# Optimization experiments

Hardware: AMD Instinct MI355X
Metric: run time of the kernel (lower is better)

Reference implementation:

```python
import jax, jax.numpy as jnp
import numpy as np

EPS = 1e-8

def _div(n, d):
    # div_with_small_value: d = d if d > eps else eps
    return n / jnp.where(d > EPS, d, EPS)

def _lstm_dir(x, Wih, Whh, bih, bhh):
    # x: (B, L, I) -> (hs (B, L, H), h_last (B, H))
    B, L, _ = x.shape
    H = Whh.shape[1]
    xg = jnp.einsum('bli,gi->blg', x, Wih) + bih + bhh  # (B, L, 4H)
    def step(carry, g):
        h, c = carry
        g = g + h @ Whh.T
        i, f, gg, o = jnp.split(g, 4, axis=-1)
        c = jax.nn.sigmoid(f) * c + jax.nn.sigmoid(i) * jnp.tanh(gg)
        h = jax.nn.sigmoid(o) * jnp.tanh(c)
        return (h, c), h
    init = (jnp.zeros((B, H), x.dtype), jnp.zeros((B, H), x.dtype))
    (hT, _), hs = jax.lax.scan(step, init, jnp.swapaxes(xg, 0, 1))
    return jnp.swapaxes(hs, 0, 1), hT

def _bilstm(x, pf, pb):
    fw, fwT = _lstm_dir(x, *pf)
    bw_r, bwT = _lstm_dir(x[:, ::-1], *pb)
    return fw, bw_r[:, ::-1], fwT, bwT

def _mp_full(v1, v2, w):
    # v1 (B,L,H); v2 (B,H) or (B,L,H); w (P,H) -> (B,L,P)
    wv1 = v1[:, :, None, :] * w                      # (B,L,P,H)
    if v2.ndim == 2:
        wv2 = v2[:, None, None, :] * w               # (B,1,P,H)
    else:
        wv2 = v2[:, :, None, :] * w                  # (B,L,P,H)
    num = jnp.sum(wv1 * wv2, -1)
    den = jnp.linalg.norm(wv1, axis=-1) * jnp.linalg.norm(wv2, axis=-1)
    return num / jnp.maximum(den, EPS)               # torch cosine_similarity eps

def _mp_pairwise(v1, v2, w):
    # v1 (B,L1,H), v2 (B,L2,H), w (P,H) -> (B,L1,L2,P)
    wv1 = w[None, :, None, :] * v1[:, None]          # (B,P,L1,H)
    wv2 = w[None, :, None, :] * v2[:, None]          # (B,P,L2,H)
    n = jnp.einsum('bpld,bpmd->bplm', wv1, wv2)
    d = jnp.linalg.norm(wv1, axis=-1)[..., :, None] * jnp.linalg.norm(wv2, axis=-1)[..., None, :]
    return jnp.transpose(_div(n, d), (0, 2, 3, 1))

def _attention(v1, v2):
    # cosine similarity matrix (B, L1, L2)
    n = jnp.einsum('bld,bmd->blm', v1, v2)
    d = jnp.linalg.norm(v1, axis=-1)[:, :, None] * jnp.linalg.norm(v2, axis=-1)[:, None, :]
    return _div(n, d)

def _forward(emb, cWih_f, cWhh_f, cbih_f, cbhh_f, cWih_b, cWhh_b, cbih_b, cbhh_b,
             aWih_f, aWhh_f, abih_f, abhh_f, aWih_b, aWhh_b, abih_b, abhh_b,
             mp_w1, mp_w2, mp_w3, mp_w4, mp_w5, mp_w6, mp_w7, mp_w8,
             fc1_W, fc1_b, fc2_W, fc2_b, text_a, text_b):
    p = emb[text_a]
    h = emb[text_b]
    cpf_p = (cWih_f, cWhh_f, cbih_f, cbhh_f)
    cpb_p = (cWih_b, cWhh_b, cbih_b, cbhh_b)
    con_p_fw, con_p_bw, _, _ = _bilstm(p, cpf_p, cpb_p)
    con_h_fw, con_h_bw, _, _ = _bilstm(h, cpf_p, cpb_p)
    # full matching
    mv_p_full_fw = _mp_full(con_p_fw, con_h_fw[:, -1], mp_w1)
    mv_p_full_bw = _mp_full(con_p_bw, con_h_bw[:, 0], mp_w2)
    mv_h_full_fw = _mp_full(con_h_fw, con_p_fw[:, -1], mp_w1)
    mv_h_full_bw = _mp_full(con_h_bw, con_p_bw[:, 0], mp_w2)
    # maxpool matching
    mv_max_fw = _mp_pairwise(con_p_fw, con_h_fw, mp_w3)
    mv_max_bw = _mp_pairwise(con_p_bw, con_h_bw, mp_w4)
    mv_p_max_fw = mv_max_fw.max(2); mv_p_max_bw = mv_max_bw.max(2)
    mv_h_max_fw = mv_max_fw.max(1); mv_h_max_bw = mv_max_bw.max(1)
    # attentive matching
    att_fw = _attention(con_p_fw, con_h_fw)          # (B,L1,L2)
    att_bw = _attention(con_p_bw, con_h_bw)
    att_h_fw = con_h_fw[:, None] * att_fw[..., None]     # (B,L1,L2,H)
    att_h_bw = con_h_bw[:, None] * att_bw[..., None]
    att_p_fw = con_p_fw[:, :, None] * att_fw[..., None]  # (B,L1,L2,H)
    att_p_bw = con_p_bw[:, :, None] * att_bw[..., None]
    att_mean_h_fw = _div(att_h_fw.sum(2), att_fw.sum(2, keepdims=True))
    att_mean_h_bw = _div(att_h_bw.sum(2), att_bw.sum(2, keepdims=True))
    att_mean_p_fw = _div(att_p_fw.sum(1), jnp.swapaxes(att_fw.sum(1, keepdims=True), 1, 2))
    att_mean_p_bw = _div(att_p_bw.sum(1), jnp.swapaxes(att_bw.sum(1, keepdims=True), 1, 2))
    mv_p_att_mean_fw = _mp_full(con_p_fw, att_mean_h_fw, mp_w5)
    mv_p_att_mean_bw = _mp_full(con_p_bw, att_mean_h_bw, mp_w6)
    mv_h_att_mean_fw = _mp_full(con_h_fw, att_mean_p_fw, mp_w5)
    mv_h_att_mean_bw = _mp_full(con_h_bw, att_mean_p_bw, mp_w6)
    att_max_h_fw = att_h_fw.max(2); att_max_h_bw = att_h_bw.max(2)
    att_max_p_fw = att_p_fw.max(1); att_max_p_bw = att_p_bw.max(1)
    mv_p_att_max_fw = _mp_full(con_p_fw, att_max_h_fw, mp_w7)
    mv_p_att_max_bw = _mp_full(con_p_bw, att_max_h_bw, mp_w8)
    mv_h_att_max_fw = _mp_full(con_h_fw, att_max_p_fw, mp_w7)
    mv_h_att_max_bw = _mp_full(con_h_bw, att_max_p_bw, mp_w8)
    mv_p = jnp.concatenate([mv_p_full_fw, mv_p_max_fw, mv_p_att_mean_fw, mv_p_att_max_fw,
                            mv_p_full_bw, mv_p_max_bw, mv_p_att_mean_bw, mv_p_att_max_bw], 2)
    mv_h = jnp.concatenate([mv_h_full_fw, mv_h_max_fw, mv_h_att_mean_fw, mv_h_att_max_fw,
                            mv_h_full_bw, mv_h_max_bw, mv_h_att_mean_bw, mv_h_att_max_bw], 2)
    apf = (aWih_f, aWhh_f, abih_f, abhh_f)
    apb = (aWih_b, aWhh_b, abih_b, abhh_b)
    _, _, p_fwT, p_bwT = _bilstm(mv_p, apf, apb)
    _, _, h_fwT, h_bwT = _bilstm(mv_h, apf, apb)
    x = jnp.concatenate([p_fwT, p_bwT, h_fwT, h_bwT], 1)  # (B, 4H)
    x = jnp.tanh(x @ fc1_W.T + fc1_b)
    return x @ fc2_W.T + fc2_b

def setup_inputs() -> dict:
    key = jax.random.key(0)
    ks = jax.random.split(key, 40)
    B, L, V, E, H, P = 16, 128, 30000, 300, 128, 4
    def n(i, shape, s=0.05):
        return jax.random.normal(ks[i], shape, jnp.float32) * s
    inp = {
        'text_a': jax.random.randint(ks[0], (B, L), 0, V, jnp.int32),
        'text_b': jax.random.randint(ks[1], (B, L), 0, V, jnp.int32),
        'emb': n(2, (V, E), 0.1),
        'cWih_f': n(3, (4*H, E)), 'cWhh_f': n(4, (4*H, H)), 'cbih_f': n(5, (4*H,)), 'cbhh_f': n(6, (4*H,)),
        'cWih_b': n(7, (4*H, E)), 'cWhh_b': n(8, (4*H, H)), 'cbih_b': n(9, (4*H,)), 'cbhh_b': n(10, (4*H,)),
        'aWih_f': n(11, (4*H, 8*P)), 'aWhh_f': n(12, (4*H, H)), 'abih_f': n(13, (4*H,)), 'abhh_f': n(14, (4*H,)),
        'aWih_b': n(15, (4*H, 8*P)), 'aWhh_b': n(16, (4*H, H)), 'abih_b': n(17, (4*H,)), 'abhh_b': n(18, (4*H,)),
        'fc1_W': n(19, (2*H, 4*H)), 'fc1_b': n(20, (2*H,)),
        'fc2_W': n(21, (2, 2*H)), 'fc2_b': n(22, (2,)),
    }
    for i in range(1, 9):
        inp[f'mp_w{i}'] = jax.random.uniform(ks[22 + i], (P, H), jnp.float32)
    return inp

def reference(text_a, text_b, emb, cWih_f, cWhh_f, cbih_f, cbhh_f, cWih_b, cWhh_b, cbih_b, cbhh_b,
              aWih_f, aWhh_f, abih_f, abhh_f, aWih_b, aWhh_b, abih_b, abhh_b,
              fc1_W, fc1_b, fc2_W, fc2_b, mp_w1, mp_w2, mp_w3, mp_w4, mp_w5, mp_w6, mp_w7, mp_w8):
    return _forward(emb, cWih_f, cWhh_f, cbih_f, cbhh_f, cWih_b, cWhh_b, cbih_b, cbhh_b,
                    aWih_f, aWhh_f, abih_f, abhh_f, aWih_b, aWhh_b, abih_b, abhh_b,
                    mp_w1, mp_w2, mp_w3, mp_w4, mp_w5, mp_w6, mp_w7, mp_w8,
                    fc1_W, fc1_b, fc2_W, fc2_b, text_a, text_b)
```

## Files before the change

kernel.cpp:

```cpp
#include <hip/hip_runtime.h>

#define B_ 16
#define L_ 128
#define ML_ 2048
#define E_ 300
#define H_ 128
#define G_ 512
#define EPSV 1e-8f

typedef const float* fp;
typedef __attribute__((ext_vector_type(2))) float f32x2;

__device__ __forceinline__ float sigm(float x) { return 1.f / (1.f + __expf(-x)); }
__device__ __forceinline__ float tanh_f(float x) {
  float e = __expf(-2.f * fabsf(x));
  float r = (1.f - e) / (1.f + e);
  return copysignf(r, x);
}
__device__ __forceinline__ float ddiv(float n, float d) {
  return n / (d > EPSV ? d : EPSV);
}
__device__ __forceinline__ void pkfma(f32x2& d, f32x2 a, f32x2 b) {
  asm("v_pk_fma_f32 %0, %1, %2, %0" : "+v"(d) : "v"(a), "v"(b));
}

__global__ __launch_bounds__(256) void k_proj(
    fp __restrict__ emb,
    const int* __restrict__ ta, const int* __restrict__ tb,
    fp Wf, fp Wb, fp bihf, fp bhhf, fp bihb, fp bhhb,
    float* __restrict__ xg)
{
  const int z = blockIdx.z;
  const int* txt = (z >> 1) ? tb : ta;
  fp W = (z & 1) ? Wb : Wf;
  fp bih = (z & 1) ? bihb : bihf;
  fp bhh = (z & 1) ? bhhb : bhhf;
  float* out = xg + (size_t)z * ML_ * G_;
  const int m0 = blockIdx.x * 64, n0 = blockIdx.y * 64;
  __shared__ float As[12][64];
  __shared__ float Bs[12][64];
  __shared__ int rowidx[64];
  const int tid = threadIdx.x;
  if (tid < 64) rowidx[tid] = txt[m0 + tid];
  __syncthreads();
  const int tm = tid >> 4, tn = tid & 15;
  float acc[4][4] = {};
  for (int k0 = 0; k0 < 300; k0 += 12) {
    for (int i = tid; i < 768; i += 256) {
      int m = i / 12, k = i - m * 12;
      As[k][m] = emb[(size_t)rowidx[m] * 300 + k0 + k];
    }
    for (int i = tid; i < 768; i += 256) {
      int n = i / 12, k = i - n * 12;
      Bs[k][n] = W[(size_t)(n0 + n) * 300 + k0 + k];
    }
    __syncthreads();
    #pragma unroll
    for (int k = 0; k < 12; ++k) {
      float4 a = *(const float4*)&As[k][tm * 4];
      float4 bv = *(const float4*)&Bs[k][tn * 4];
      float aa[4] = {a.x, a.y, a.z, a.w};
      #pragma unroll
      for (int i = 0; i < 4; ++i) {
        acc[i][0] = fmaf(aa[i], bv.x, acc[i][0]);
        acc[i][1] = fmaf(aa[i], bv.y, acc[i][1]);
        acc[i][2] = fmaf(aa[i], bv.z, acc[i][2]);
        acc[i][3] = fmaf(aa[i], bv.w, acc[i][3]);
      }
    }
    __syncthreads();
  }
  float biasv[4];
  #pragma unroll
  for (int j = 0; j < 4; ++j)
    biasv[j] = bih[n0 + tn * 4 + j] + bhh[n0 + tn * 4 + j];
  #pragma unroll
  for (int i = 0; i < 4; ++i) {
    float* row = out + (size_t)(m0 + tm * 4 + i) * G_ + n0 + tn * 4;
    #pragma unroll
    for (int j = 0; j < 4; ++j) row[j] = acc[i][j] + biasv[j];
  }
}

__global__ __launch_bounds__(512, 2) void k_lstm(
    fp __restrict__ xg, fp Whhf, fp Whhb, float* __restrict__ out)
{
  const int b = blockIdx.x, z = blockIdx.y, dir = z & 1;
  fp Whh = dir ? Whhb : Whhf;
  fp __restrict__ xgz = xg + ((size_t)z * ML_ + (size_t)b * L_) * G_;
  float* __restrict__ outz = out + ((size_t)z * ML_ + (size_t)b * L_) * H_;
  const int tid = threadIdx.x;
  const int wv = tid >> 6, l = tid & 63;
  const int kh = l & 3, rg = l >> 2;
  const int j = wv * 16 + rg;
  const int b0 = kh & 1, b1 = (kh >> 1) & 1;
  float4 wq[4][8];
  #pragma unroll
  for (int g = 0; g < 4; ++g) {
    const float4* p = (const float4*)(Whh + (size_t)(g * 128 + j) * H_ + kh * 32);
    #pragma unroll
    for (int q = 0; q < 8; ++q) wq[g][q] = p[q];
  }
  __shared__ float hs[2][128];
  if (tid < 128) hs[0][tid] = 0.f;
  float c = 0.f;
  const int pos0 = dir ? (L_ - 1) : 0;
  float xv = xgz[(size_t)pos0 * G_ + kh * 128 + j];
  __syncthreads();
  int cur = 0;
  for (int t = 0; t < L_; ++t) {
    const int pos = dir ? (L_ - 1 - t) : t;
    const int tnx = (t + 1 < L_) ? (t + 1) : t;
    const int posn = dir ? (L_ - 1 - tnx) : tnx;
    float xvn = xgz[(size_t)posn * G_ + kh * 128 + j];
    f32x2 a2[4];
    #pragma unroll
    for (int g = 0; g < 4; ++g) { a2[g].x = 0.f; a2[g].y = 0.f; }
    const float4* h4 = (const float4*)(&hs[cur][kh * 32]);
    #pragma unroll
    for (int q = 0; q < 8; ++q) {
      float4 hv = h4[q];
      f32x2 hlo; hlo.x = hv.x; hlo.y = hv.y;
      f32x2 hhi; hhi.x = hv.z; hhi.y = hv.w;
      #pragma unroll
      for (int g = 0; g < 4; ++g) {
        float4 wqv = wq[g][q];
        f32x2 wlo; wlo.x = wqv.x; wlo.y = wqv.y;
        f32x2 whi; whi.x = wqv.z; whi.y = wqv.w;
        pkfma(a2[g], wlo, hlo);
        pkfma(a2[g], whi, hhi);
      }
    }
    float pg0 = a2[0].x + a2[0].y;
    float pg1 = a2[1].x + a2[1].y;
    float pg2 = a2[2].x + a2[2].y;
    float pg3 = a2[3].x + a2[3].y;
    float sendA = b0 ? pg0 : pg1;
    float sendB = b0 ? pg2 : pg3;
    float keepA = b0 ? pg1 : pg0;
    float keepB = b0 ? pg3 : pg2;
    float uA = keepA + __shfl_xor(sendA, 1, 64);
    float uB = keepB + __shfl_xor(sendB, 1, 64);
    float mine  = b1 ? uB : uA;
    float send2 = b1 ? uA : uB;
    float tot = mine + __shfl_xor(send2, 2, 64);
    float pre = tot + xv;
    float act = (kh == 2) ? tanh_f(pre) : sigm(pre);
    float e1 = __shfl_xor(act, 1, 64);
    float e2 = __shfl_xor(act, 2, 64);
    float e3 = __shfl_xor(e1, 2, 64);
    float iv = (kh == 0) ? act : (kh == 1) ? e1 : (kh == 2) ? e2 : e3;
    float fv = (kh == 0) ? e1 : (kh == 1) ? act : (kh == 2) ? e3 : e2;
    float gv = (kh == 0) ? e2 : (kh == 1) ? e3 : (kh == 2) ? act : e1;
    float ov = (kh == 0) ? e3 : (kh == 1) ? e2 : (kh == 2) ? e1 : act;
    c = fmaf(fv, c, iv * gv);
    float hn = ov * tanh_f(c);
    const int nxt = cur ^ 1;
    if (kh == 0) {
      hs[nxt][j] = hn;
      outz[(size_t)pos * H_ + j] = hn;
    }
    asm volatile("s_waitcnt lgkmcnt(0)" ::: "memory");
    __builtin_amdgcn_s_barrier();
    cur = nxt; xv = xvn;
  }
}

__global__ __launch_bounds__(256) void k_att(
    fp __restrict__ con, fp w3, fp w4,
    float* __restrict__ att, float* __restrict__ ameanh, float* __restrict__ amaxh,
    float* __restrict__ pcpart, float* __restrict__ mv)
{
  const int b = blockIdx.x, dir = blockIdx.y, lt = blockIdx.z;
  const int l0 = lt * 32;
  fp __restrict__ cp = con + ((size_t)dir * B_ + b) * L_ * H_;
  fp __restrict__ ch = con + ((size_t)(2 + dir) * B_ + b) * L_ * H_;
  fp w = dir ? w4 : w3;
  float* __restrict__ attg = att + ((size_t)dir * B_ + b) * L_ * L_;
  __shared__ float cps[32][132];
  __shared__ float chs[32][132];
  __shared__ float w2s[4][128];
  __shared__ float attb[32][33];
  __shared__ float pcb[4][32][33];
  __shared__ float n0l[32], nql[4][32], n0m[32], nqm[4][32], asum_s[32];
  const int tid = threadIdx.x;
  for (int i = tid; i < 512; i += 256) {
    float wv = w[i];
    w2s[i >> 7][i & 127] = wv * wv;
  }
  for (int i = tid; i < 4096; i += 256)
    cps[i >> 7][i & 127] = cp[(size_t)(l0 + (i >> 7)) * H_ + (i & 127)];
  __syncthreads();
  for (int d = tid; d < 160; d += 256) {
    int l = d / 5, q = d - l * 5;
    const float4* vr = (const float4*)&cps[l][0];
    float s = 0.f;
    if (q == 0) {
      #pragma unroll 8
      for (int h4 = 0; h4 < 32; ++h4) {
        float4 v = vr[h4];
        s += v.x*v.x + v.y*v.y + v.z*v.z + v.w*v.w;
      }
      n0l[l] = sqrtf(s);
    } else {
      const float4* wr = (const float4*)&w2s[q - 1][0];
      #pragma unroll 8
      for (int h4 = 0; h4 < 32; ++h4) {
        float4 v = vr[h4]; float4 ww = wr[h4];
        s += v.x*v.x*ww.x + v.y*v.y*ww.y + v.z*v.z*ww.z + v.w*v.w*ww.w;
      }
      nql[q - 1][l] = sqrtf(s);
    }
  }
  const int tl = tid >> 3, t8 = tid & 7;
  float amean_acc[16], amax_acc[16];
  #pragma unroll
  for (int i = 0; i < 16; ++i) { amean_acc[i] = 0.f; amax_acc[i] = -3.4e38f; }
  float asum_reg = 0.f;
  float pmax_reg = -3.4e38f;
  for (int mc = 0; mc < 4; ++mc) {
    __syncthreads();
    for (int i = tid; i < 4096; i += 256)
      chs[i >> 7][i & 127] = ch[(size_t)(mc * 32 + (i >> 7)) * H_ + (i & 127)];
    __syncthreads();
    for (int d = tid; d < 160; d += 256) {
      int m = d / 5, q = d - m * 5;
      const float4* vr = (const float4*)&chs[m][0];
      float s = 0.f;
      if (q == 0) {
        #pragma unroll 8
        for (int h4 = 0; h4 < 32; ++h4) {
          float4 v = vr[h4];
          s += v.x*v.x + v.y*v.y + v.z*v.z + v.w*v.w;
        }
        n0m[m] = sqrtf(s);
      } else {
        const float4* wr = (const float4*)&w2s[q - 1][0];
        #pragma unroll 8
        for (int h4 = 0; h4 < 32; ++h4) {
          float4 v = vr[h4]; float4 ww = wr[h4];
          s += v.x*v.x*ww.x + v.y*v.y*ww.y + v.z*v.z*ww.z + v.w*v.w*ww.w;
        }
        nqm[q - 1][m] = sqrtf(s);
      }
    }
    __syncthreads();
    float a0[4], ap0[4], ap1[4], ap2[4], ap3[4];
    #pragma unroll
    for (int mm = 0; mm < 4; ++mm) { a0[mm]=0.f; ap0[mm]=0.f; ap1[mm]=0.f; ap2[mm]=0.f; ap3[mm]=0.f; }
    #pragma unroll 4
    for (int h4 = 0; h4 < 32; ++h4) {
      const float4 av = *(const float4*)&cps[tl][h4 * 4];
      const float4 q0 = *(const float4*)&w2s[0][h4 * 4];
      const float4 q1 = *(const float4*)&w2s[1][h4 * 4];
      const float4 q2 = *(const float4*)&w2s[2][h4 * 4];
      const float4 q3 = *(const float4*)&w2s[3][h4 * 4];
      #pragma unroll
      for (int mm = 0; mm < 4; ++mm) {
        const float4 cv = *(const float4*)&chs[t8 * 4 + mm][h4 * 4];
        float px = av.x * cv.x, py = av.y * cv.y, pz = av.z * cv.z, pw = av.w * cv.w;
        a0[mm] += (px + py) + (pz + pw);
        ap0[mm] += px * q0.x + py * q0.y + pz * q0.z + pw * q0.w;
        ap1[mm] += px * q1.x + py * q1.y + pz * q1.z + pw * q1.w;
        ap2[mm] += px * q2.x + py * q2.y + pz * q2.z + pw * q2.w;
        ap3[mm] += px * q3.x + py * q3.y + pz * q3.z + pw * q3.w;
      }
    }
    #pragma unroll
    for (int mm = 0; mm < 4; ++mm) {
      const int m = t8 * 4 + mm;
      float attv = ddiv(a0[mm], n0l[tl] * n0m[m]);
      attb[tl][m] = attv;
      attg[(size_t)(l0 + tl) * L_ + mc * 32 + m] = attv;
      pcb[0][tl][m] = ddiv(ap0[mm], nql[0][tl] * nqm[0][m]);
      pcb[1][tl][m] = ddiv(ap1[mm], nql[1][tl] * nqm[1][m]);
      pcb[2][tl][m] = ddiv(ap2[mm], nql[2][tl] * nqm[2][m]);
      pcb[3][tl][m] = ddiv(ap3[mm], nql[3][tl] * nqm[3][m]);
    }
    __syncthreads();
    for (int mq = 0; mq < 32; ++mq) {
      float avv = attb[tl][mq];
      const float4* cr = (const float4*)&chs[mq][t8 * 16];
      #pragma unroll
      for (int i = 0; i < 4; ++i) {
        float4 cv = cr[i];
        float t0 = avv * cv.x, t1 = avv * cv.y, t2 = avv * cv.z, t3 = avv * cv.w;
        amean_acc[4*i+0] += t0; amax_acc[4*i+0] = fmaxf(amax_acc[4*i+0], t0);
        amean_acc[4*i+1] += t1; amax_acc[4*i+1] = fmaxf(amax_acc[4*i+1], t1);
        amean_acc[4*i+2] += t2; amax_acc[4*i+2] = fmaxf(amax_acc[4*i+2], t2);
        amean_acc[4*i+3] += t3; amax_acc[4*i+3] = fmaxf(amax_acc[4*i+3], t3);
      }
    }
    if (tid < 32) {
      float s = 0.f;
      for (int mq = 0; mq < 32; ++mq) s += attb[tid][mq];
      asum_reg += s;
    }
    if (tid < 128) {
      const int p = tid >> 5, q = tid & 31;
      float mx = pmax_reg;
      for (int mq = 0; mq < 32; ++mq) mx = fmaxf(mx, pcb[p][q][mq]);
      pmax_reg = mx;
      float mx2 = -3.4e38f;
      for (int lq = 0; lq < 32; ++lq) mx2 = fmaxf(mx2, pcb[p][lq][q]);
      pcpart[((((size_t)dir * B_ + b) * 4 + lt) * 4 + p) * L_ + mc * 32 + q] = mx2;
    }
    __syncthreads();
  }
  if (tid < 32) asum_s[tid] = asum_reg;
  __syncthreads();
  {
    float den = asum_s[tl]; den = (den > EPSV) ? den : EPSV;
    const size_t base = (((size_t)dir * B_ + b) * L_ + l0 + tl) * H_ + t8 * 16;
    #pragma unroll
    for (int i = 0; i < 16; ++i) {
      ameanh[base + i] = amean_acc[i] / den;
      amaxh[base + i] = amax_acc[i];
    }
  }
  if (tid < 128) {
    const int p = tid >> 5, lq = tid & 31;
    mv[(size_t)(b * L_ + l0 + lq) * 32 + (dir ? 20 : 4) + p] = pmax_reg;
  }
}

__global__ __launch_bounds__(256) void k_col(
    fp __restrict__ con, fp __restrict__ att,
    fp __restrict__ pcpart,
    float* __restrict__ ameanp, float* __restrict__ amaxp, float* __restrict__ mv)
{
  const int b = blockIdx.x, dir = blockIdx.y, mt = blockIdx.z;
  const int m0 = mt * 32;
  fp __restrict__ cp = con + ((size_t)dir * B_ + b) * L_ * H_;
  fp __restrict__ attg = att + ((size_t)dir * B_ + b) * L_ * L_;
  __shared__ float atts[128][33];
  __shared__ float cpc[32][132];
  __shared__ float asum_s[32];
  const int tid = threadIdx.x;
  for (int i = tid; i < 4096; i += 256)
    atts[i >> 5][i & 31] = attg[(size_t)(i >> 5) * L_ + m0 + (i & 31)];
  __syncthreads();
  if (tid < 32) {
    float s = 0.f;
    for (int l = 0; l < 128; ++l) s += atts[l][tid];
    asum_s[tid] = s;
  }
  const int tm = tid >> 3, t8 = tid & 7;
  float mean_acc[16], max_acc[16];
  #pragma unroll
  for (int i = 0; i < 16; ++i) { mean_acc[i] = 0.f; max_acc[i] = -3.4e38f; }
  for (int lc = 0; lc < 4; ++lc) {
    __syncthreads();
    for (int i = tid; i < 4096; i += 256)
      cpc[i >> 7][i & 127] = cp[(size_t)(lc * 32 + (i >> 7)) * H_ + (i & 127)];
    __syncthreads();
    for (int lq = 0; lq < 32; ++lq) {
      float avv = atts[lc * 32 + lq][tm];
      const float4* cr = (const float4*)&cpc[lq][t8 * 16];
      #pragma unroll
      for (int i = 0; i < 4; ++i) {
        float4 cv = cr[i];
        float t0 = avv * cv.x, t1 = avv * cv.y, t2 = avv * cv.z, t3 = avv * cv.w;
        mean_acc[4*i+0] += t0; max_acc[4*i+0] = fmaxf(max_acc[4*i+0], t0);
        mean_acc[4*i+1] += t1; max_acc[4*i+1] = fmaxf(max_acc[4*i+1], t1);
        mean_acc[4*i+2] += t2; max_acc[4*i+2] = fmaxf(max_acc[4*i+2], t2);
        mean_acc[4*i+3] += t3; max_acc[4*i+3] = fmaxf(max_acc[4*i+3], t3);
      }
    }
  }
  __syncthreads();
  {
    float den = asum_s[tm]; den = (den > EPSV) ? den : EPSV;
    const size_t base = (((size_t)dir * B_ + b) * L_ + m0 + tm) * H_ + t8 * 16;
    #pragma unroll
    for (int i = 0; i < 16; ++i) {
      ameanp[base + i] = mean_acc[i] / den;
      amaxp[base + i] = max_acc[i];
    }
  }
  if (tid < 128) {
    const int p = tid >> 5, mq = tid & 31;
    float mx = -3.4e38f;
    #pragma unroll
    for (int lt = 0; lt < 4; ++lt)
      mx = fmaxf(mx, pcpart[((((size_t)dir * B_ + b) * 4 + lt) * 4 + p) * L_ + m0 + mq]);
    mv[(size_t)(ML_ + b * L_ + m0 + mq) * 32 + (dir ? 20 : 4) + p] = mx;
  }
}

__global__ __launch_bounds__(256) void k_mv(
    fp __restrict__ con,
    fp __restrict__ ameanh, fp __restrict__ amaxh,
    fp __restrict__ ameanp, fp __restrict__ amaxp,
    fp w1, fp w2, fp w5, fp w6, fp w7, fp w8,
    float* __restrict__ mv)
{
  int idx = blockIdx.x * 256 + threadIdx.x;
  const int p = idx & 3; int t1 = idx >> 2;
  const int type = t1 % 3; int t2 = t1 / 3;
  const int dir = t2 & 1; int t3 = t2 >> 1;
  const int l = t3 & 127; int t4 = t3 >> 7;
  const int b = t4 & 15; const int side = t4 >> 4;
  const float* v1 = con + (((size_t)(side ? 2 : 0) + dir) * B_ + b) * L_ * H_ + (size_t)l * H_;
  const float* v2;
  if (type == 0) {
    v2 = con + (((size_t)(side ? 0 : 2) + dir) * B_ + b) * L_ * H_ + (size_t)(dir ? 0 : L_ - 1) * H_;
  } else {
    const float* base = (type == 1) ? (side ? ameanp : ameanh) : (side ? amaxp : amaxh);
    v2 = base + (((size_t)dir * B_ + b) * L_ + l) * H_;
  }
  fp w = (type == 0) ? (dir ? w2 : w1) : (type == 1) ? (dir ? w6 : w5) : (dir ? w8 : w7);
  w += p * H_;
  float num = 0.f, s1 = 0.f, s2 = 0.f;
  for (int h = 0; h < H_; ++h) {
    float wv = w[h];
    float a = v1[h] * wv, bb = v2[h] * wv;
    num = fmaf(a, bb, num);
    s1 = fmaf(a, a, s1);
    s2 = fmaf(bb, bb, s2);
  }
  float den = sqrtf(s1) * sqrtf(s2);
  int slot = (type == 0) ? (dir ? 16 : 0) + p : (type == 1) ? (dir ? 24 : 8) + p : (dir ? 28 : 12) + p;
  mv[((size_t)side * ML_ + b * L_ + l) * 32 + slot] = ddiv(num, den);
}

__global__ __launch_bounds__(256) void k_aggproj(
    fp __restrict__ mv,
    fp Wf, fp Wb, fp bihf, fp bhhf, fp bihb, fp bhhb,
    float* __restrict__ xg)
{
  const int z = blockIdx.y, side = z >> 1, dir = z & 1;
  fp W = dir ? Wb : Wf;
  fp bih = dir ? bihb : bihf;
  fp bhh = dir ? bhhb : bhhf;
  const int r0 = blockIdx.x * 8;
  const float* src = mv + ((size_t)side * ML_ + r0) * 32;
  float* out = xg + ((size_t)z * ML_ + r0) * G_;
  __shared__ float mvs[8][32];
  const int tid = threadIdx.x;
  mvs[tid >> 5][tid & 31] = src[tid];
  __syncthreads();
  float w0[32], w1v[32];
  {
    const float4* wp = (const float4*)(W + (size_t)tid * 32);
    #pragma unroll
    for (int q = 0; q < 8; ++q) {
      float4 u = wp[q];
      w0[4*q+0] = u.x; w0[4*q+1] = u.y; w0[4*q+2] = u.z; w0[4*q+3] = u.w;
    }
    const float4* wp2 = (const float4*)(W + (size_t)(tid + 256) * 32);
    #pragma unroll
    for (int q = 0; q < 8; ++q) {
      float4 u = wp2[q];
      w1v[4*q+0] = u.x; w1v[4*q+1] = u.y; w1v[4*q+2] = u.z; w1v[4*q+3] = u.w;
    }
  }
  float bias0 = bih[tid] + bhh[tid];
  float bias1 = bih[tid + 256] + bhh[tid + 256];
  for (int r = 0; r < 8; ++r) {
    float acc0 = bias0, acc1 = bias1;
    #pragma unroll
    for (int k = 0; k < 32; ++k) {
      float xv = mvs[r][k];
      acc0 = fmaf(w0[k], xv, acc0);
      acc1 = fmaf(w1v[k], xv, acc1);
    }
    out[(size_t)r * G_ + tid] = acc0;
    out[(size_t)r * G_ + tid + 256] = acc1;
  }
}

__global__ __launch_bounds__(256) void k_fc(
    fp __restrict__ aggseq,
    fp fc1W, fp fc1b, fp fc2W, fp fc2b,
    float* __restrict__ out)
{
  const int b = blockIdx.x, tid = threadIdx.x;
  __shared__ float x[512];
  __shared__ float y[256];
  for (int i = tid; i < 512; i += 256) {
    int z = i >> 7, h = i & 127;
    int l = (z & 1) ? 0 : (L_ - 1);
    x[i] = aggseq[(((size_t)z * B_ + b) * L_ + l) * H_ + h];
  }
  __syncthreads();
  {
    float acc = fc1b[tid];
    const float4* wr = (const float4*)(fc1W + (size_t)tid * 512);
    const float4* x4 = (const float4*)x;
    #pragma unroll 8
    for (int k4 = 0; k4 < 128; ++k4) {
      float4 u = wr[k4];
      float4 xv = x4[k4];
      acc = fmaf(u.x, xv.x, acc);
      acc = fmaf(u.y, xv.y, acc);
      acc = fmaf(u.z, xv.z, acc);
      acc = fmaf(u.w, xv.w, acc);
    }
    y[tid] = tanh_f(acc);
  }
  __syncthreads();
  if (tid < 2) {
    float acc = fc2b[tid];
    for (int k = 0; k < 256; ++k) acc = fmaf(fc2W[tid * 256 + k], y[k], acc);
    out[b * 2 + tid] = acc;
  }
}

extern "C" void kernel_launch(void* const* d_in, const int* in_sizes, int n_in,
                              void* d_out, int out_size, void* d_ws, size_t ws_size,
                              hipStream_t stream) {
  (void)in_sizes; (void)n_in; (void)out_size; (void)ws_size;
  const int* ta = (const int*)d_in[0];
  const int* tb = (const int*)d_in[1];
  fp emb   = (fp)d_in[2];
  fp cWihf = (fp)d_in[3];
  fp cWhhf = (fp)d_in[4];
  fp cbihf = (fp)d_in[5];
  fp cbhhf = (fp)d_in[6];
  fp cWihb = (fp)d_in[7];
  fp cWhhb = (fp)d_in[8];
  fp cbihb = (fp)d_in[9];
  fp cbhhb = (fp)d_in[10];
  fp aWihf = (fp)d_in[11];
  fp aWhhf = (fp)d_in[12];
  fp abihf = (fp)d_in[13];
  fp abhhf = (fp)d_in[14];
  fp aWihb = (fp)d_in[15];
  fp aWhhb = (fp)d_in[16];
  fp abihb = (fp)d_in[17];
  fp abhhb = (fp)d_in[18];
  fp fc1W  = (fp)d_in[19];
  fp fc1b  = (fp)d_in[20];
  fp fc2W  = (fp)d_in[21];
  fp fc2b  = (fp)d_in[22];
  fp w1 = (fp)d_in[23];
  fp w2 = (fp)d_in[24];
  fp w3 = (fp)d_in[25];
  fp w4 = (fp)d_in[26];
  fp w5 = (fp)d_in[27];
  fp w6 = (fp)d_in[28];
  fp w7 = (fp)d_in[29];
  fp w8 = (fp)d_in[30];

  float* ws = (float*)d_ws;
  float* xg     = ws;
  float* con    = xg     + (size_t)4 * ML_ * G_;
  float* attw   = con    + (size_t)4 * ML_ * H_;
  float* ameanh = attw   + (size_t)2 * B_ * L_ * L_;
  float* amaxh  = ameanh + (size_t)2 * ML_ * H_;
  float* ameanp = amaxh  + (size_t)2 * ML_ * H_;
  float* amaxp  = ameanp + (size_t)2 * ML_ * H_;
  float* pcpart = amaxp  + (size_t)2 * ML_ * H_;
  float* mvb    = pcpart + (size_t)2 * B_ * 16 * L_;
  float* aggseq = mvb    + (size_t)2 * ML_ * 32;

  k_proj<<<dim3(32, 8, 4), 256, 0, stream>>>(emb, ta, tb, cWihf, cWihb,
                                             cbihf, cbhhf, cbihb, cbhhb, xg);
  k_lstm<<<dim3(16, 4), 512, 0, stream>>>(xg, cWhhf, cWhhb, con);
  k_att<<<dim3(16, 2, 4), 256, 0, stream>>>(con, w3, w4, attw, ameanh, amaxh, pcpart, mvb);
  k_col<<<dim3(16, 2, 4), 256, 0, stream>>>(con, attw, pcpart, ameanp, amaxp, mvb);
  k_mv<<<384, 256, 0, stream>>>(con, ameanh, amaxh, ameanp, amaxp, w1, w2, w5, w6, w7, w8, mvb);
  k_aggproj<<<dim3(256, 4), 256, 0, stream>>>(mvb, aWihf, aWihb, abihf, abhhf, abihb, abhhb, xg);
  k_lstm<<<dim3(16, 4), 512, 0, stream>>>(xg, aWhhf, aWhhb, aggseq);
  k_fc<<<16, 256, 0, stream>>>(aggseq, fc1W, fc1b, fc2W, fc2b, (float*)d_out);
}
```

Before: 479.5 us.

## Pad LDS hidden state and use butterfly reductions in the LSTM recurrence

```diff
diff --git a/kernel.cpp b/kernel.cpp
--- a/kernel.cpp
+++ b/kernel.cpp
@@ -10,6 +10,7 @@
 
 typedef const float* fp;
 typedef __attribute__((ext_vector_type(2))) float f32x2;
+typedef __attribute__((ext_vector_type(4))) float f32x4;
 
 __device__ __forceinline__ float sigm(float x) { return 1.f / (1.f + __expf(-x)); }
 __device__ __forceinline__ float tanh_f(float x) {
@@ -93,16 +94,20 @@
   const int wv = tid >> 6, l = tid & 63;
   const int kh = l & 3, rg = l >> 2;
   const int j = wv * 16 + rg;
-  const int b0 = kh & 1, b1 = (kh >> 1) & 1;
-  float4 wq[4][8];
+  f32x4 wq[4][8];
   #pragma unroll
   for (int g = 0; g < 4; ++g) {
-    const float4* p = (const float4*)(Whh + (size_t)(g * 128 + j) * H_ + kh * 32);
+    const f32x4* p = (const f32x4*)(Whh + (size_t)(g * 128 + j) * H_ + kh * 32);
     #pragma unroll
     for (int q = 0; q < 8; ++q) wq[g][q] = p[q];
   }
-  __shared__ float hs[2][128];
-  if (tid < 128) hs[0][tid] = 0.f;
+  #pragma unroll
+  for (int g = 0; g < 4; ++g) {
+    asm volatile("" : "+v"(wq[g][0]), "+v"(wq[g][1]), "+v"(wq[g][2]), "+v"(wq[g][3]),
+                      "+v"(wq[g][4]), "+v"(wq[g][5]), "+v"(wq[g][6]), "+v"(wq[g][7]));
+  }
+  __shared__ float hs[2][132];
+  if (tid < 128) hs[0][(tid >> 5) * 33 + (tid & 31)] = 0.f;
   float c = 0.f;
   const int pos0 = dir ? (L_ - 1) : 0;
   float xv = xgz[(size_t)pos0 * G_ + kh * 128 + j];
@@ -116,15 +121,15 @@
     f32x2 a2[4];
     #pragma unroll
     for (int g = 0; g < 4; ++g) { a2[g].x = 0.f; a2[g].y = 0.f; }
-    const float4* h4 = (const float4*)(&hs[cur][kh * 32]);
+    const f32x4* h4 = (const f32x4*)(&hs[cur][kh * 33]);
     #pragma unroll
     for (int q = 0; q < 8; ++q) {
-      float4 hv = h4[q];
+      f32x4 hv = h4[q];
       f32x2 hlo; hlo.x = hv.x; hlo.y = hv.y;
       f32x2 hhi; hhi.x = hv.z; hhi.y = hv.w;
       #pragma unroll
       for (int g = 0; g < 4; ++g) {
-        float4 wqv = wq[g][q];
+        f32x4 wqv = wq[g][q];
         f32x2 wlo; wlo.x = wqv.x; wlo.y = wqv.y;
         f32x2 whi; whi.x = wqv.z; whi.y = wqv.w;
         pkfma(a2[g], wlo, hlo);
@@ -135,29 +140,27 @@
     float pg1 = a2[1].x + a2[1].y;
     float pg2 = a2[2].x + a2[2].y;
     float pg3 = a2[3].x + a2[3].y;
-    float sendA = b0 ? pg0 : pg1;
-    float sendB = b0 ? pg2 : pg3;
-    float keepA = b0 ? pg1 : pg0;
-    float keepB = b0 ? pg3 : pg2;
-    float uA = keepA + __shfl_xor(sendA, 1, 64);
-    float uB = keepB + __shfl_xor(sendB, 1, 64);
-    float mine  = b1 ? uB : uA;
-    float send2 = b1 ? uA : uB;
-    float tot = mine + __shfl_xor(send2, 2, 64);
-    float pre = tot + xv;
-    float act = (kh == 2) ? tanh_f(pre) : sigm(pre);
-    float e1 = __shfl_xor(act, 1, 64);
-    float e2 = __shfl_xor(act, 2, 64);
-    float e3 = __shfl_xor(e1, 2, 64);
-    float iv = (kh == 0) ? act : (kh == 1) ? e1 : (kh == 2) ? e2 : e3;
-    float fv = (kh == 0) ? e1 : (kh == 1) ? act : (kh == 2) ? e3 : e2;
-    float gv = (kh == 0) ? e2 : (kh == 1) ? e3 : (kh == 2) ? act : e1;
-    float ov = (kh == 0) ? e3 : (kh == 1) ? e2 : (kh == 2) ? e1 : act;
+    pg0 += (kh == 0) ? xv : 0.f;
+    pg1 += (kh == 1) ? xv : 0.f;
+    pg2 += (kh == 2) ? xv : 0.f;
+    pg3 += (kh == 3) ? xv : 0.f;
+    pg0 += __shfl_xor(pg0, 1, 64);
+    pg1 += __shfl_xor(pg1, 1, 64);
+    pg2 += __shfl_xor(pg2, 1, 64);
+    pg3 += __shfl_xor(pg3, 1, 64);
+    pg0 += __shfl_xor(pg0, 2, 64);
+    pg1 += __shfl_xor(pg1, 2, 64);
+    pg2 += __shfl_xor(pg2, 2, 64);
+    pg3 += __shfl_xor(pg3, 2, 64);
+    float iv = sigm(pg0);
+    float fv = sigm(pg1);
+    float gv = tanh_f(pg2);
+    float ov = sigm(pg3);
     c = fmaf(fv, c, iv * gv);
     float hn = ov * tanh_f(c);
     const int nxt = cur ^ 1;
     if (kh == 0) {
-      hs[nxt][j] = hn;
+      hs[nxt][(j >> 5) * 33 + (j & 31)] = hn;
       outz[(size_t)pos * H_ + j] = hn;
     }
     asm volatile("s_waitcnt lgkmcnt(0)" ::: "memory");
```

Result: slower. 840.1 us (+75.2%).
